# Optimization experiments

Hardware: AMD Instinct MI355X
Metric: run time of the kernel (lower is better)

The kernel has to match this reference:

```python
import jax, jax.numpy as jnp
import numpy as np

N = 100000   # nodes
E = 1600000  # edges (nnz of sparse A)
H = 128      # hidden_size


def _row_normalize(x):
    # F.normalize(x, p=1, dim=1): divide each row by max(L1 norm, 1e-12); zero-out infs
    norm = jnp.sum(jnp.abs(x), axis=1, keepdims=True)
    y = x / jnp.maximum(norm, 1e-12)
    return jnp.where(jnp.isinf(y), 0.0, y)


def setup_inputs() -> dict:
    key = jax.random.key(0)
    k = jax.random.split(key, 7)
    x = jax.random.normal(k[0], (N, H), dtype=jnp.float32)
    A_rows = jax.random.randint(k[1], (E,), 0, N, dtype=jnp.int32)
    A_cols = jax.random.randint(k[2], (E,), 0, N, dtype=jnp.int32)
    A_vals = jax.random.uniform(k[3], (E,), dtype=jnp.float32)
    W = jax.random.normal(k[4], (H, H), dtype=jnp.float32) / np.float32(np.sqrt(H))
    b = jax.random.normal(k[5], (H,), dtype=jnp.float32) * 0.01
    time_step = jax.random.uniform(k[6], (1,), dtype=jnp.float32)
    return {"x": x, "A_rows": A_rows, "A_cols": A_cols, "A_vals": A_vals,
            "W": W, "b": b, "time_step": time_step}


def reference(x, A_rows, A_cols, A_vals, W, b, time_step):
    shortcut = x
    xn = _row_normalize(x)                       # normalize=True
    # sparse.mm(A, x): gather neighbor rows, scale by edge value, scatter-add to dst rows
    msgs = A_vals[:, None] * xn[A_cols]          # [E, H]
    f = jax.ops.segment_sum(msgs, A_rows, num_segments=N)  # [N, H]
    f = f @ W.T + b                              # time_varying=True linear
    # dropout p=0 -> identity (eval semantics)
    f = _row_normalize(f)                        # normalize=True
    f = jnp.maximum(f, 0.0)                      # relu
    return shortcut + f * time_step[0]           # Euler residual with learned step
```

## Files before the change

kernel.cpp:

```cpp
#include <hip/hip_runtime.h>

constexpr int HD = 128;
constexpr int BROWS = 64;
constexpr int CAP = 2048;
constexpr int NBMAX = 2048;
constexpr int EPB = 16384;
constexpr int SLOT_STRIDE = 4096;
constexpr int SLOT_BYTES = 32768;

typedef __attribute__((ext_vector_type(8))) short short8v;
typedef __attribute__((ext_vector_type(4))) float f32x4;
typedef __attribute__((ext_vector_type(2))) float f32x2;

__device__ __forceinline__ int rl(int v, int j) {
    return __builtin_amdgcn_readlane(v, j);
}
__device__ __forceinline__ float rlf(int v, int j) {
    return __uint_as_float((unsigned)__builtin_amdgcn_readlane(v, j));
}
__device__ __forceinline__ unsigned f2bf(float f) {
    unsigned u = __float_as_uint(f);
    return (u + 0x7fffu + ((u >> 16) & 1u)) >> 16;
}
__device__ __forceinline__ f32x2 bf2f(unsigned u) {
    f32x2 r = {__uint_as_float(u << 16), __uint_as_float(u & 0xffff0000u)};
    return r;
}

#define META_OFF_MASK 0x03FFFF00

__global__ void prep_kernel(const float* __restrict__ x,
                            unsigned* __restrict__ xb,
                            float* __restrict__ xnorm,
                            const float* __restrict__ W,
                            unsigned* __restrict__ Wb,
                            int* __restrict__ cursor,
                            int N, int PB, int NB) {
    int bid = blockIdx.x;
    int tid = threadIdx.x;
    if (bid < PB) {
        int wid = tid >> 6;
        int lane = tid & 63;
        int row = bid * 8 + wid * 2 + (lane >> 5);
        if (row >= N) return;
        int l32 = lane & 31;
        float4 v = *((const float4*)(x + (size_t)row * HD) + l32);
        float s = fabsf(v.x) + fabsf(v.y) + fabsf(v.z) + fabsf(v.w);
        s += __shfl_xor(s, 1, 64);
        s += __shfl_xor(s, 2, 64);
        s += __shfl_xor(s, 4, 64);
        s += __shfl_xor(s, 8, 64);
        s += __shfl_xor(s, 16, 64);
        float nm = fmaxf(s, 1e-12f);
        float rn = 1.0f / nm;
        if (l32 == 0) xnorm[row] = nm;
        uint2 pk;
        pk.x = f2bf(v.x * rn) | (f2bf(v.y * rn) << 16);
        pk.y = f2bf(v.z * rn) | (f2bf(v.w * rn) << 16);
        *((uint2*)(xb + (size_t)row * 64) + l32) = pk;
    } else if (bid < PB + 32) {
        int t = (bid - PB) * 256 + tid;
        int col = t >> 6, k2 = t & 63;
        float w0 = W[col * HD + 2 * k2];
        float w1 = W[col * HD + 2 * k2 + 1];
        unsigned pk = f2bf(w0) | (f2bf(w1) << 16);
        int byte = (col * 256 + k2 * 4) ^ ((col & 7) << 4);
        *(unsigned*)((char*)Wb + byte) = pk;
    } else {
        for (int i = tid; i < NB; i += 256) cursor[i] = 0;
    }
}

__global__ void __launch_bounds__(512) scatter_kernel(
    const int* __restrict__ rows, const int* __restrict__ cols,
    const float* __restrict__ vals, int* __restrict__ cursor,
    int2* __restrict__ outslots, int2* __restrict__ lastslot, int E, int NB) {
    int tid = threadIdx.x;
    if (NB <= NBMAX) {
        __shared__ int lbin[NBMAX];
        __shared__ int lbase[NBMAX];
        __shared__ unsigned short rk16[EPB];
        for (int i = tid; i < NBMAX; i += 512) lbin[i] = 0;
        __syncthreads();
        const int4* rows4 = (const int4*)rows;
        int E4 = E >> 2;
        int base4 = blockIdx.x * (EPB / 4);
#pragma unroll
        for (int i = 0; i < 8; ++i) {
            int e4 = base4 + i * 512 + tid;
            if (e4 < E4) {
                int4 r = rows4[e4];
                int li = (i * 512 + tid) * 4;
                rk16[li + 0] = (unsigned short)atomicAdd(&lbin[r.x >> 6], 1);
                rk16[li + 1] = (unsigned short)atomicAdd(&lbin[r.y >> 6], 1);
                rk16[li + 2] = (unsigned short)atomicAdd(&lbin[r.z >> 6], 1);
                rk16[li + 3] = (unsigned short)atomicAdd(&lbin[r.w >> 6], 1);
            }
        }
        __syncthreads();
        for (int i = tid; i < NB; i += 512) {
            int c = lbin[i];
            if (c) lbase[i] = atomicAdd(&cursor[i], c);
        }
        __syncthreads();
        const int4* cols4 = (const int4*)cols;
        const float4* vals4 = (const float4*)vals;
#pragma unroll
        for (int i = 0; i < 8; ++i) {
            int e4 = base4 + i * 512 + tid;
            if (e4 < E4) {
                int4 r4 = rows4[e4];
                int4 c4 = cols4[e4];
                float4 v4 = vals4[e4];
                int li = (i * 512 + tid) * 4;
                int ra[4] = {r4.x, r4.y, r4.z, r4.w};
                int ca[4] = {c4.x, c4.y, c4.z, c4.w};
                float va[4] = {v4.x, v4.y, v4.z, v4.w};
#pragma unroll
                for (int k = 0; k < 4; ++k) {
                    int r = ra[k];
                    int bkt = r >> 6;
                    int idx = lbase[bkt] + rk16[li + k];
                    if (idx < CAP) {
                        int2* sp = (bkt == NB - 1)
                                       ? lastslot
                                       : outslots + (size_t)bkt * SLOT_STRIDE;
                        sp[idx] = make_int2((ca[k] << 8) | ((r & 63) << 26),
                                            __float_as_int(va[k]));
                    }
                }
            }
        }
        if (blockIdx.x == 0) {
            for (int e = (E & ~3) + tid; e < E; e += 512) {
                int r = rows[e];
                int bkt = r >> 6;
                int rel = atomicAdd(&cursor[bkt], 1);
                if (rel < CAP) {
                    int2* sp = (bkt == NB - 1)
                                   ? lastslot
                                   : outslots + (size_t)bkt * SLOT_STRIDE;
                    sp[rel] = make_int2((cols[e] << 8) | ((r & 63) << 26),
                                        __float_as_int(vals[e]));
                }
            }
        }
    } else {
        int base = blockIdx.x * EPB;
        for (int i = 0; i < 32; ++i) {
            int e = base + i * 512 + tid;
            if (e >= E) break;
            int r = rows[e];
            int bkt = r >> 6;
            int rel = atomicAdd(&cursor[bkt], 1);
            if (rel < CAP) {
                int2* sp = (bkt == NB - 1)
                               ? lastslot
                               : outslots + (size_t)bkt * SLOT_STRIDE;
                sp[rel] = make_int2((cols[e] << 8) | ((r & 63) << 26),
                                    __float_as_int(vals[e]));
            }
        }
    }
}

__global__ void __launch_bounds__(1024) mega_kernel(
    const unsigned* __restrict__ xb, const float* __restrict__ xnorm,
    const int* __restrict__ cursor, const int2* __restrict__ lastslot,
    const unsigned* __restrict__ Wb, const float* __restrict__ bias,
    const float* __restrict__ tsp, float* out, int N, int NB) {
    __shared__ char wb_raw[HD * HD * 2];
    __shared__ char fb_raw[BROWS * HD * 2];
    __shared__ int2 sorted[CAP];
    __shared__ int lcnt[BROWS], lbeg[BROWS], lcur[BROWS];
    __shared__ float rowsum[BROWS];

    int tid = threadIdx.x;
    int bid = blockIdx.x;
    const int2* slot = (bid == NB - 1)
                           ? lastslot
                           : (const int2*)((const char*)out +
                                           (size_t)bid * SLOT_BYTES);
    int ct = cursor[bid];
    if (ct > CAP) ct = CAP;

    if (tid < BROWS) lcnt[tid] = 0;

    int2 m0 = make_int2(0, 0), m1 = make_int2(0, 0);
    bool e0 = tid < ct, e1 = tid + 1024 < ct;
    if (e0) m0 = slot[tid];
    if (e1) m1 = slot[tid + 1024];
    __syncthreads();

    if (e0) atomicAdd(&lcnt[(unsigned)m0.x >> 26], 1);
    if (e1) atomicAdd(&lcnt[(unsigned)m1.x >> 26], 1);
    __syncthreads();

    if (tid < 64) {
        int c = lcnt[tid];
        int s = c;
#pragma unroll
        for (int m = 1; m < 64; m <<= 1) {
            int t2 = __shfl_up(s, m, 64);
            if (tid >= m) s += t2;
        }
        lbeg[tid] = s - c;
        lcur[tid] = s - c;
    }
    __syncthreads();

    if (e0) {
        int p = atomicAdd(&lcur[(unsigned)m0.x >> 26], 1);
        if (p < CAP) sorted[p] = m0;
    }
    if (e1) {
        int p = atomicAdd(&lcur[(unsigned)m1.x >> 26], 1);
        if (p < CAP) sorted[p] = m1;
    }
    {
        const float4* s4 = (const float4*)Wb;
        float4* d4 = (float4*)wb_raw;
        for (int i = tid; i < HD * HD * 2 / 16; i += 1024) d4[i] = s4[i];
    }
    __syncthreads();

    int lane = tid & 63;
    int wid = tid >> 6;
    int half = lane >> 5;
    int l32 = lane & 31;
    float ts = tsp[0];
    const char* xb2 = (const char*)xb + (l32 << 3);

    float a0[4], a1[4], a2[4], a3[4];
#pragma unroll
    for (int rr = 0; rr < 4; ++rr) {
        int lr = wid * 4 + rr;
        int beg = lbeg[lr], cnt = lcnt[lr];
        f32x2 p01 = {0.f, 0.f}, p23 = {0.f, 0.f};
        f32x2 q01 = {0.f, 0.f}, q23 = {0.f, 0.f};
        for (int jb = 0; jb < cnt; jb += 64) {
            int rem = cnt - jb;
            if (rem > 64) rem = 64;
            int2 meta = make_int2(0, 0);
            if (lane < rem) meta = sorted[beg + jb + lane];
            int jn = (rem + 1) >> 1;
            int j = 0;
            for (; j + 2 <= jn; j += 2) {
                int oa0 = rl(meta.x, 2 * j) & META_OFF_MASK;
                int oa1 = rl(meta.x, 2 * j + 1) & META_OFF_MASK;
                int ob0 = rl(meta.x, 2 * j + 2) & META_OFF_MASK;
                int ob1 = rl(meta.x, 2 * j + 3) & META_OFF_MASK;
                float sa0 = rlf(meta.y, 2 * j), sa1 = rlf(meta.y, 2 * j + 1);
                float sb0 = rlf(meta.y, 2 * j + 2), sb1 = rlf(meta.y, 2 * j + 3);
                int oa = half ? oa1 : oa0;
                int ob = half ? ob1 : ob0;
                float sa = half ? sa1 : sa0;
                float sb = half ? sb1 : sb0;
                uint2 ua = *(const uint2*)(xb2 + oa);
                uint2 ub = *(const uint2*)(xb2 + ob);
                p01 += bf2f(ua.x) * sa;
                p23 += bf2f(ua.y) * sa;
                q01 += bf2f(ub.x) * sb;
                q23 += bf2f(ub.y) * sb;
            }
            for (; j < jn; ++j) {
                int o0 = rl(meta.x, 2 * j) & META_OFF_MASK;
                int o1 = rl(meta.x, 2 * j + 1) & META_OFF_MASK;
                float s0 = rlf(meta.y, 2 * j), s1 = rlf(meta.y, 2 * j + 1);
                int o = half ? o1 : o0;
                float s = half ? s1 : s0;
                uint2 u = *(const uint2*)(xb2 + o);
                p01 += bf2f(u.x) * s;
                p23 += bf2f(u.y) * s;
            }
        }
        p01 += q01;
        p23 += q23;
        a0[rr] = p01.x;
        a1[rr] = p01.y;
        a2[rr] = p23.x;
        a3[rr] = p23.y;
    }
#pragma unroll
    for (int rr = 0; rr < 4; ++rr) {
        a0[rr] += __shfl_xor(a0[rr], 32, 64);
        a1[rr] += __shfl_xor(a1[rr], 32, 64);
        a2[rr] += __shfl_xor(a2[rr], 32, 64);
        a3[rr] += __shfl_xor(a3[rr], 32, 64);
    }

    if (half == 0) {
#pragma unroll
        for (int rr = 0; rr < 4; ++rr) {
            int row = wid * 4 + rr;
            uint2 pk;
            pk.x = f2bf(a0[rr]) | (f2bf(a1[rr]) << 16);
            pk.y = f2bf(a2[rr]) | (f2bf(a3[rr]) << 16);
            int byte = (row * 256 + l32 * 8) ^ ((row & 7) << 4);
            *(uint2*)(fb_raw + byte) = pk;
        }
    }
    if (tid < BROWS) rowsum[tid] = 0.f;
    __syncthreads();

    int rt = wid >> 2;
    int ct0 = (wid & 3) * 2;
    int c = lane & 15;
    int kg = lane >> 4;
    int arow = rt * 16 + c;
    int bcol0 = ct0 * 16 + c;
    int bcol1 = bcol0 + 16;
    f32x4 acc0 = {0.f, 0.f, 0.f, 0.f}, acc1 = {0.f, 0.f, 0.f, 0.f};
#pragma unroll
    for (int kk = 0; kk < 4; ++kk) {
        int ka = kg * 16 + kk * 64;
        short8v af = *(const short8v*)(fb_raw +
                                       ((arow * 256 + ka) ^ ((arow & 7) << 4)));
        short8v bf0 = *(const short8v*)(wb_raw +
                                        ((bcol0 * 256 + ka) ^ ((bcol0 & 7) << 4)));
        short8v bf1 = *(const short8v*)(wb_raw +
                                        ((bcol1 * 256 + ka) ^ ((bcol1 & 7) << 4)));
        acc0 = __builtin_amdgcn_mfma_f32_16x16x32_bf16(af, bf0, acc0, 0, 0, 0);
        acc1 = __builtin_amdgcn_mfma_f32_16x16x32_bf16(af, bf1, acc1, 0, 0, 0);
    }

    float bias0 = bias[bcol0];
    float bias1 = bias[bcol1];
    float g0r[4], g1r[4];
#pragma unroll
    for (int r = 0; r < 4; ++r) {
        float v0 = acc0[r] + bias0;
        float v1 = acc1[r] + bias1;
        g0r[r] = v0;
        g1r[r] = v1;
        float s = fabsf(v0) + fabsf(v1);
        s += __shfl_xor(s, 1, 64);
        s += __shfl_xor(s, 2, 64);
        s += __shfl_xor(s, 4, 64);
        s += __shfl_xor(s, 8, 64);
        if (c == 0) atomicAdd(&rowsum[rt * 16 + kg * 4 + r], s);
    }
    __syncthreads();
#pragma unroll
    for (int r = 0; r < 4; ++r) {
        int lrow = rt * 16 + kg * 4 + r;
        int row = bid * BROWS + lrow;
        if (row < N) {
            float rn = 1.0f / fmaxf(rowsum[lrow], 1e-12f);
            float G0 = fmaxf(g0r[r] * rn, 0.f);
            float G1 = fmaxf(g1r[r] * rn, 0.f);
            float nm = xnorm[row];
            unsigned u0 = xb[(size_t)row * 64 + ct0 * 8 + (c >> 1)];
            unsigned u1 = xb[(size_t)row * 64 + ct0 * 8 + 8 + (c >> 1)];
            unsigned h0 = (c & 1) ? (u0 & 0xffff0000u) : (u0 << 16);
            unsigned h1 = (c & 1) ? (u1 & 0xffff0000u) : (u1 << 16);
            float x0 = __uint_as_float(h0) * nm;
            float x1 = __uint_as_float(h1) * nm;
            out[(size_t)row * HD + bcol0] = fmaf(ts, G0, x0);
            out[(size_t)row * HD + bcol1] = fmaf(ts, G1, x1);
        }
    }
}

extern "C" void kernel_launch(void* const* d_in, const int* in_sizes, int n_in,
                              void* d_out, int out_size, void* d_ws,
                              size_t ws_size, hipStream_t stream) {
    const float* x = (const float*)d_in[0];
    const int* Ar = (const int*)d_in[1];
    const int* Ac = (const int*)d_in[2];
    const float* Av = (const float*)d_in[3];
    const float* W = (const float*)d_in[4];
    const float* b = (const float*)d_in[5];
    const float* ts = (const float*)d_in[6];

    int N = in_sizes[0] / HD;
    int E = in_sizes[1];
    float* out = (float*)d_out;

    int NB = (N + BROWS - 1) / BROWS;

    char* ws = (char*)d_ws;
    size_t o = 0;
    auto take = [&](size_t bytes) {
        void* p = ws + o;
        o += (bytes + 511) & ~(size_t)511;
        return p;
    };
    int* cursor = (int*)take((size_t)NB * 4);
    float* xnorm = (float*)take((size_t)N * 4);
    unsigned* Wb = (unsigned*)take((size_t)HD * HD * 2);
    int2* lastslot = (int2*)take((size_t)CAP * 8);
    unsigned* xb = (unsigned*)take((size_t)N * 64 * 4);

    int PB = (N + 7) / 8;
    int SB = (E + EPB - 1) / EPB;

    prep_kernel<<<PB + 33, 256, 0, stream>>>(x, xb, xnorm, W, Wb, cursor, N, PB,
                                             NB);
    scatter_kernel<<<SB, 512, 0, stream>>>(Ar, Ac, Av, cursor, (int2*)d_out,
                                           lastslot, E, NB);
    mega_kernel<<<NB, 1024, 0, stream>>>(xb, xnorm, cursor, lastslot, Wb, b, ts,
                                         out, N, NB);
}
```

Baseline: 127.5 us.

## Fuse normalization prep and edge bucketing into one build kernel

Merges the row-normalize/bf16 pack, W packing, and the edge-scatter bucketing into a single 512-thread kernel whose block ranges handle each role, with cursor zeroing moved to a tiny separate init kernel. The scatter part now uses smaller edge chunks per block (EPB 16384 to 4096), keeps per-edge rank and payload in registers instead of a shared rk16 array, and reads rows/cols/vals only once. The goal is to overlap the independent prep and scatter work, cut a full kernel boundary, and remove the second read of the row indices. The trade-off is more blocks doing global atomics on cursor and a mixed-role grid whose shared-memory footprint applies to every block.

```diff
diff --git a/kernel.cpp b/kernel.cpp
--- a/kernel.cpp
+++ b/kernel.cpp
@@ -4,7 +4,7 @@
 constexpr int BROWS = 64;
 constexpr int CAP = 2048;
 constexpr int NBMAX = 2048;
-constexpr int EPB = 16384;
+constexpr int EPB = 4096;
 constexpr int SLOT_STRIDE = 4096;
 constexpr int SLOT_BYTES = 32768;
 
@@ -29,19 +29,26 @@
 
 #define META_OFF_MASK 0x03FFFF00
 
-__global__ void prep_kernel(const float* __restrict__ x,
-                            unsigned* __restrict__ xb,
-                            float* __restrict__ xnorm,
-                            const float* __restrict__ W,
-                            unsigned* __restrict__ Wb,
-                            int* __restrict__ cursor,
-                            int N, int PB, int NB) {
+__global__ void init_kernel(int* __restrict__ cursor, int NB) {
+    int i = blockIdx.x * 1024 + threadIdx.x;
+    if (i < NB) cursor[i] = 0;
+}
+
+__global__ void __launch_bounds__(512) build_kernel(
+    const float* __restrict__ x, unsigned* __restrict__ xb,
+    float* __restrict__ xnorm, const float* __restrict__ W,
+    unsigned* __restrict__ Wb, const int* __restrict__ rows,
+    const int* __restrict__ cols, const float* __restrict__ vals,
+    int* __restrict__ cursor, int2* __restrict__ outslots,
+    int2* __restrict__ lastslot, int N, int E, int PB, int NB) {
+    __shared__ int lbin[NBMAX];
+    __shared__ int lbase[NBMAX];
     int bid = blockIdx.x;
     int tid = threadIdx.x;
     if (bid < PB) {
         int wid = tid >> 6;
         int lane = tid & 63;
-        int row = bid * 8 + wid * 2 + (lane >> 5);
+        int row = bid * 16 + wid * 2 + (lane >> 5);
         if (row >= N) return;
         int l32 = lane & 31;
         float4 v = *((const float4*)(x + (size_t)row * HD) + l32);
@@ -58,8 +65,8 @@
         pk.x = f2bf(v.x * rn) | (f2bf(v.y * rn) << 16);
         pk.y = f2bf(v.z * rn) | (f2bf(v.w * rn) << 16);
         *((uint2*)(xb + (size_t)row * 64) + l32) = pk;
-    } else if (bid < PB + 32) {
-        int t = (bid - PB) * 256 + tid;
+    } else if (bid < PB + 16) {
+        int t = (bid - PB) * 512 + tid;
         int col = t >> 6, k2 = t & 63;
         float w0 = W[col * HD + 2 * k2];
         float w1 = W[col * HD + 2 * k2 + 1];
@@ -67,98 +74,86 @@
         int byte = (col * 256 + k2 * 4) ^ ((col & 7) << 4);
         *(unsigned*)((char*)Wb + byte) = pk;
     } else {
-        for (int i = tid; i < NB; i += 256) cursor[i] = 0;
-    }
-}
-
-__global__ void __launch_bounds__(512) scatter_kernel(
-    const int* __restrict__ rows, const int* __restrict__ cols,
-    const float* __restrict__ vals, int* __restrict__ cursor,
-    int2* __restrict__ outslots, int2* __restrict__ lastslot, int E, int NB) {
-    int tid = threadIdx.x;
-    if (NB <= NBMAX) {
-        __shared__ int lbin[NBMAX];
-        __shared__ int lbase[NBMAX];
-        __shared__ unsigned short rk16[EPB];
-        for (int i = tid; i < NBMAX; i += 512) lbin[i] = 0;
-        __syncthreads();
-        const int4* rows4 = (const int4*)rows;
-        int E4 = E >> 2;
-        int base4 = blockIdx.x * (EPB / 4);
-#pragma unroll
-        for (int i = 0; i < 8; ++i) {
-            int e4 = base4 + i * 512 + tid;
-            if (e4 < E4) {
-                int4 r = rows4[e4];
-                int li = (i * 512 + tid) * 4;
-                rk16[li + 0] = (unsigned short)atomicAdd(&lbin[r.x >> 6], 1);
-                rk16[li + 1] = (unsigned short)atomicAdd(&lbin[r.y >> 6], 1);
-                rk16[li + 2] = (unsigned short)atomicAdd(&lbin[r.z >> 6], 1);
-                rk16[li + 3] = (unsigned short)atomicAdd(&lbin[r.w >> 6], 1);
-            }
-        }
-        __syncthreads();
-        for (int i = tid; i < NB; i += 512) {
-            int c = lbin[i];
-            if (c) lbase[i] = atomicAdd(&cursor[i], c);
-        }
-        __syncthreads();
-        const int4* cols4 = (const int4*)cols;
-        const float4* vals4 = (const float4*)vals;
-#pragma unroll
-        for (int i = 0; i < 8; ++i) {
-            int e4 = base4 + i * 512 + tid;
-            if (e4 < E4) {
-                int4 r4 = rows4[e4];
-                int4 c4 = cols4[e4];
-                float4 v4 = vals4[e4];
-                int li = (i * 512 + tid) * 4;
+        int sb = bid - PB - 16;
+        if (NB <= NBMAX) {
+            for (int i = tid; i < NBMAX; i += 512) lbin[i] = 0;
+            __syncthreads();
+            const int4* rows4 = (const int4*)rows;
+            const int4* cols4 = (const int4*)cols;
+            const float4* vals4 = (const float4*)vals;
+            int E4 = E >> 2;
+            int base4 = sb * (EPB / 4);
+            int mx[8], vv[8], bkt[8], rk[8];
+#pragma unroll
+            for (int i = 0; i < 2; ++i) {
+                int e4 = base4 + i * 512 + tid;
+                bool ok = e4 < E4;
+                int4 r4 = ok ? rows4[e4] : make_int4(0, 0, 0, 0);
+                int4 c4 = ok ? cols4[e4] : make_int4(0, 0, 0, 0);
+                float4 v4 = ok ? vals4[e4] : make_float4(0, 0, 0, 0);
                 int ra[4] = {r4.x, r4.y, r4.z, r4.w};
                 int ca[4] = {c4.x, c4.y, c4.z, c4.w};
                 float va[4] = {v4.x, v4.y, v4.z, v4.w};
 #pragma unroll
                 for (int k = 0; k < 4; ++k) {
-                    int r = ra[k];
-                    int bkt = r >> 6;
-                    int idx = lbase[bkt] + rk16[li + k];
-                    if (idx < CAP) {
-                        int2* sp = (bkt == NB - 1)
-                                       ? lastslot
-                                       : outslots + (size_t)bkt * SLOT_STRIDE;
-                        sp[idx] = make_int2((ca[k] << 8) | ((r & 63) << 26),
-                                            __float_as_int(va[k]));
+                    int ii = i * 4 + k;
+                    bkt[ii] = -1;
+                    if (ok) {
+                        int r = ra[k];
+                        mx[ii] = (ca[k] << 8) | ((r & 63) << 26);
+                        vv[ii] = __float_as_int(va[k]);
+                        bkt[ii] = r >> 6;
+                        rk[ii] = atomicAdd(&lbin[bkt[ii]], 1);
                     }
                 }
             }
-        }
-        if (blockIdx.x == 0) {
-            for (int e = (E & ~3) + tid; e < E; e += 512) {
+            __syncthreads();
+            for (int i = tid; i < NB; i += 512) {
+                int c = lbin[i];
+                if (c) lbase[i] = atomicAdd(&cursor[i], c);
+            }
+            __syncthreads();
+#pragma unroll
+            for (int ii = 0; ii < 8; ++ii) {
+                if (bkt[ii] >= 0) {
+                    int idx = lbase[bkt[ii]] + rk[ii];
+                    if (idx < CAP) {
+                        int2* sp = (bkt[ii] == NB - 1)
+                                       ? lastslot
+                                       : outslots + (size_t)bkt[ii] * SLOT_STRIDE;
+                        sp[idx] = make_int2(mx[ii], vv[ii]);
+                    }
+                }
+            }
+            if (sb == 0) {
+                for (int e = (E & ~3) + tid; e < E; e += 512) {
+                    int r = rows[e];
+                    int bk = r >> 6;
+                    int rel = atomicAdd(&cursor[bk], 1);
+                    if (rel < CAP) {
+                        int2* sp = (bk == NB - 1)
+                                       ? lastslot
+                                       : outslots + (size_t)bk * SLOT_STRIDE;
+                        sp[rel] = make_int2((cols[e] << 8) | ((r & 63) << 26),
+                                            __float_as_int(vals[e]));
+                    }
+                }
+            }
+        } else {
+            int base = sb * EPB;
+            for (int i = 0; i < 8; ++i) {
+                int e = base + i * 512 + tid;
+                if (e >= E) break;
                 int r = rows[e];
-                int bkt = r >> 6;
-                int rel = atomicAdd(&cursor[bkt], 1);
+                int bk = r >> 6;
+                int rel = atomicAdd(&cursor[bk], 1);
                 if (rel < CAP) {
-                    int2* sp = (bkt == NB - 1)
+                    int2* sp = (bk == NB - 1)
                                    ? lastslot
-                                   : outslots + (size_t)bkt * SLOT_STRIDE;
+                                   : outslots + (size_t)bk * SLOT_STRIDE;
                     sp[rel] = make_int2((cols[e] << 8) | ((r & 63) << 26),
                                         __float_as_int(vals[e]));
                 }
-            }
-        }
-    } else {
-        int base = blockIdx.x * EPB;
-        for (int i = 0; i < 32; ++i) {
-            int e = base + i * 512 + tid;
-            if (e >= E) break;
-            int r = rows[e];
-            int bkt = r >> 6;
-            int rel = atomicAdd(&cursor[bkt], 1);
-            if (rel < CAP) {
-                int2* sp = (bkt == NB - 1)
-                               ? lastslot
-                               : outslots + (size_t)bkt * SLOT_STRIDE;
-                sp[rel] = make_int2((cols[e] << 8) | ((r & 63) << 26),
-                                    __float_as_int(vals[e]));
             }
         }
     }
@@ -392,13 +387,13 @@
     int2* lastslot = (int2*)take((size_t)CAP * 8);
     unsigned* xb = (unsigned*)take((size_t)N * 64 * 4);
 
-    int PB = (N + 7) / 8;
+    int PB = (N + 15) / 16;
     int SB = (E + EPB - 1) / EPB;
 
-    prep_kernel<<<PB + 33, 256, 0, stream>>>(x, xb, xnorm, W, Wb, cursor, N, PB,
-                                             NB);
-    scatter_kernel<<<SB, 512, 0, stream>>>(Ar, Ac, Av, cursor, (int2*)d_out,
-                                           lastslot, E, NB);
+    init_kernel<<<(NB + 1023) / 1024, 1024, 0, stream>>>(cursor, NB);
+    build_kernel<<<PB + 16 + SB, 512, 0, stream>>>(
+        x, xb, xnorm, W, Wb, Ar, Ac, Av, cursor, (int2*)d_out, lastslot, N, E,
+        PB, NB);
     mega_kernel<<<NB, 1024, 0, stream>>>(xb, xnorm, cursor, lastslot, Wb, b, ts,
                                          out, N, NB);
 }
```

New measurement: 132.4 us. +3.8%, slower.
